# Kernel tuning notes

Measured on AMD Instinct MI355X. Metric: run time of the kernel, lower is better.

The kernel has to match this reference:

```python
import jax, jax.numpy as jnp
import numpy as np

B, S, H, I, E, TOP_K, NS = 2, 2048, 2048, 1408, 8, 2, 2
SI = I * NS  # shared expert intermediate (intermediate_size * num_shared_expert)
INIT = 0.02


def setup_inputs() -> dict:
    key = jax.random.key(0)
    ks = jax.random.split(key, 9)
    f32 = jnp.float32
    return {
        "hidden_states": jax.random.normal(ks[0], (B, S, H), f32),
        # router classifier: Linear(H, E, bias=False), torch weight [E, H]
        "router_w": (jax.random.normal(ks[1], (E, H), f32) * INIT),
        # grouped experts (SwiGLU, no bias): [E, H, I], [E, H, I], [E, I, H]
        "gate_w": (jax.random.normal(ks[2], (E, H, I), f32) * INIT),
        "up_w": (jax.random.normal(ks[3], (E, H, I), f32) * INIT),
        "down_w": (jax.random.normal(ks[4], (E, I, H), f32) * INIT),
        # shared expert _MLP (bias=True), stored in matmul orientation
        "s_gate_w": (jax.random.normal(ks[5], (H, SI), f32) * INIT),
        "s_gate_b": jnp.zeros((SI,), f32),
        "s_up_w": (jax.random.normal(ks[6], (H, SI), f32) * INIT),
        "s_up_b": jnp.zeros((SI,), f32),
        "s_down_w": (jax.random.normal(ks[7], (SI, H), f32) * INIT),
        "s_down_b": jnp.zeros((H,), f32),
    }


def reference(hidden_states, router_w, gate_w, up_w, down_w,
              s_gate_w, s_gate_b, s_up_w, s_up_b, s_down_w, s_down_b):
    b, s, h = hidden_states.shape
    x = hidden_states.reshape(-1, h)          # [T, H]
    T = x.shape[0]
    num_experts = router_w.shape[0]

    # ---- router: logits -> fp32 softmax -> top-k -> renormalize ----
    logits = x @ router_w.T                   # [T, E]
    probs = jax.nn.softmax(logits.astype(jnp.float32), axis=-1)
    topk_w, topk_idx = jax.lax.top_k(probs, TOP_K)            # [T, K]
    topk_w = topk_w / jnp.sum(topk_w, axis=-1, keepdims=True)
    # dense combine weights [T, E]; zero for unrouted experts
    combine = jnp.zeros((T, num_experts), probs.dtype)
    combine = combine.at[jnp.arange(T)[:, None], topk_idx].add(topk_w)

    # ---- grouped SwiGLU experts; scan over E keeps peak memory at [T, I] ----
    def expert_step(acc, ws):
        gw, uw, dw, ce = ws                  # [H,I], [H,I], [I,H], [T]
        out = (jax.nn.silu(x @ gw) * (x @ uw)) @ dw           # [T, H]
        return acc + ce[:, None].astype(out.dtype) * out, None

    moe_out, _ = jax.lax.scan(expert_step, jnp.zeros_like(x),
                              (gate_w, up_w, down_w, combine.T))

    # ---- shared expert SwiGLU MLP (bias=True), overlapped -> added ----
    shared = (jax.nn.silu(x @ s_gate_w + s_gate_b)
              * (x @ s_up_w + s_up_b)) @ s_down_w + s_down_b

    return (moe_out + shared).reshape(b, s, h)
```

## Files before the change

### kernel.cpp

```cpp
#include <hip/hip_runtime.h>
#include <hip/hip_bf16.h>
#include <stdint.h>

#define T_TOK 4096
#define HDIM  2048
#define IDIM  1408
#define NEXP  8
#define SIDIM 2816
#define GU_CAP 781
#define DN_CAP 440

typedef __bf16 bf16_t;
typedef __bf16 bf16x8 __attribute__((ext_vector_type(8)));
typedef __bf16 bf16x4 __attribute__((ext_vector_type(4)));
typedef float  f32x4  __attribute__((ext_vector_type(4)));

typedef uint32_t __attribute__((address_space(3))) lds_u32;
typedef uint32_t __attribute__((address_space(1))) glb_u32;

__device__ __forceinline__ void glds16(const bf16_t* g, const char* l) {
  __builtin_amdgcn_global_load_lds((const glb_u32*)g, (lds_u32*)l, 16, 0, 0);
}

__device__ __forceinline__ void bar() {
  asm volatile("" ::: "memory");
  __builtin_amdgcn_s_barrier();
  asm volatile("" ::: "memory");
}
#define VMW4 asm volatile("s_waitcnt vmcnt(4)" ::: "memory")
#define VMW0 asm volatile("s_waitcnt vmcnt(0)" ::: "memory")

__device__ __forceinline__ int xcd_swz(int orig, int nwg) {
  int q = nwg >> 3, r = nwg & 7;
  int x = orig & 7, i = orig >> 3;
  return (x < r ? x * (q + 1) : r * (q + 1) + (x - r) * q) + i;
}

__global__ void tcvt_kernel(const float* __restrict__ in, bf16_t* __restrict__ out, int R, int C) {
  in  += (size_t)blockIdx.z * R * C;
  out += (size_t)blockIdx.z * R * C;
  __shared__ bf16_t tb[64][72];
  const int r0 = blockIdx.y * 64, c0 = blockIdx.x * 64;
  const int tid = threadIdx.x;
  const int cf4 = tid & 15, rr = tid >> 4;
#pragma unroll
  for (int s = 0; s < 4; ++s) {
    int r = rr + 16 * s;
    float4 v = *(const float4*)(in + (size_t)(r0 + r) * C + c0 + cf4 * 4);
    tb[cf4 * 4 + 0][r] = (bf16_t)v.x;
    tb[cf4 * 4 + 1][r] = (bf16_t)v.y;
    tb[cf4 * 4 + 2][r] = (bf16_t)v.z;
    tb[cf4 * 4 + 3][r] = (bf16_t)v.w;
  }
  __syncthreads();
  const int c = tid >> 2, rb = (tid & 3) * 16;
  bf16x8 w0 = *(const bf16x8*)&tb[c][rb];
  bf16x8 w1 = *(const bf16x8*)&tb[c][rb + 8];
  bf16_t* op = out + (size_t)(c0 + c) * R + r0 + rb;
  *(bf16x8*)op = w0;
  *(bf16x8*)(op + 8) = w1;
}

__global__ void tcvt_gu_kernel(const float* __restrict__ in0, const float* __restrict__ in1,
                               bf16_t* __restrict__ out, int R, int C) {
  const int e = blockIdx.z >> 1, which = blockIdx.z & 1;
  const float* in = (which ? in1 : in0) + (size_t)e * R * C;
  out += (size_t)e * (2 * C) * R;
  __shared__ bf16_t tb[64][72];
  const int r0 = blockIdx.y * 64, c0 = blockIdx.x * 64;
  const int tid = threadIdx.x;
  const int cf4 = tid & 15, rr = tid >> 4;
#pragma unroll
  for (int s = 0; s < 4; ++s) {
    int r = rr + 16 * s;
    float4 v = *(const float4*)(in + (size_t)(r0 + r) * C + c0 + cf4 * 4);
    tb[cf4 * 4 + 0][r] = (bf16_t)v.x;
    tb[cf4 * 4 + 1][r] = (bf16_t)v.y;
    tb[cf4 * 4 + 2][r] = (bf16_t)v.z;
    tb[cf4 * 4 + 3][r] = (bf16_t)v.w;
  }
  __syncthreads();
  const int c = tid >> 2, rb = (tid & 3) * 16;
  bf16x8 w0 = *(const bf16x8*)&tb[c][rb];
  bf16x8 w1 = *(const bf16x8*)&tb[c][rb + 8];
  int cg = c0 + c;
  int nprime = ((cg >> 4) << 5) + which * 16 + (cg & 15);
  bf16_t* op = out + (size_t)nprime * R + r0 + rb;
  *(bf16x8*)op = w0;
  *(bf16x8*)(op + 8) = w1;
}

__global__ void router_kernel(const float* __restrict__ x, const float* __restrict__ rw,
                              bf16_t* __restrict__ xb,
                              int* __restrict__ tk_i, float* __restrict__ tk_w,
                              int* __restrict__ counts) {
  int gtid = blockIdx.x * 256 + threadIdx.x;
  int t = gtid >> 6, lane = gtid & 63;
  const float4* xr = (const float4*)(x + (size_t)t * HDIM);
  bf16x4* xo = (bf16x4*)(xb + (size_t)t * HDIM);
  float acc[NEXP];
#pragma unroll
  for (int e = 0; e < NEXP; e++) acc[e] = 0.f;
  for (int i = lane; i < HDIM / 4; i += 64) {
    float4 xv = xr[i];
    bf16x4 o;
    o[0] = (bf16_t)xv.x; o[1] = (bf16_t)xv.y; o[2] = (bf16_t)xv.z; o[3] = (bf16_t)xv.w;
    xo[i] = o;
#pragma unroll
    for (int e = 0; e < NEXP; e++) {
      float4 wv = ((const float4*)(rw + e * HDIM))[i];
      acc[e] += xv.x * wv.x + xv.y * wv.y + xv.z * wv.z + xv.w * wv.w;
    }
  }
#pragma unroll
  for (int e = 0; e < NEXP; e++)
#pragma unroll
    for (int off = 32; off; off >>= 1) acc[e] += __shfl_down(acc[e], off);
  if (lane == 0) {
    int i1 = 0; float m1 = acc[0];
#pragma unroll
    for (int e = 1; e < NEXP; e++) if (acc[e] > m1) { m1 = acc[e]; i1 = e; }
    int i2 = -1; float m2 = -1e30f;
#pragma unroll
    for (int e = 0; e < NEXP; e++) if (e != i1 && acc[e] > m2) { m2 = acc[e]; i2 = e; }
    float w1 = 1.f / (1.f + __expf(m2 - m1));
    tk_i[t * 2] = i1; tk_i[t * 2 + 1] = i2;
    tk_w[t * 2] = w1; tk_w[t * 2 + 1] = 1.f - w1;
    atomicAdd(&counts[i1], 1); atomicAdd(&counts[i2], 1);
  }
}

__global__ void build_kernel(int* __restrict__ meta) {
  __shared__ int snmt;
  if (threadIdx.x == 0) {
    int o = 0;
    for (int e = 0; e < NEXP; e++) { meta[16 + e] = o; o += meta[e]; }
    meta[24] = o;
    int nmt = 0;
    for (int e = 0; e < NEXP; e++) {
      int nt = (meta[e] + 255) >> 8;
      for (int i = 0; i < nt; i++) { meta[32 + nmt] = e; meta[80 + nmt] = i << 8; nmt++; }
    }
    meta[25] = nmt;
    meta[26] = nmt * 11 + 352;
    meta[27] = nmt * 8 + 128;
    snmt = nmt;
  }
  __syncthreads();
  const int nmt = snmt;
  int4* gt = (int4*)(meta + 128);
  const int ng = nmt * 11 + 352;
  for (int i = threadIdx.x; i < ng; i += 256) {
    int4 v; v.w = 0;
    if (i < nmt * 11) {
      int g = i / (nmt * 2), rem = i - g * (nmt * 2);
      int yt, xt;
      if (g < 5) { yt = rem >> 1; xt = g * 2 + (rem & 1); }
      else       { yt = rem;      xt = 10; }
      v.x = 0 | (meta[32 + yt] << 1); v.y = meta[80 + yt]; v.z = xt * 256;
    } else {
      int k = i - nmt * 11;
      int g = k >> 5, rem = k & 31;
      int yt = rem >> 1, xt = g * 2 + (rem & 1);
      v.x = 1; v.y = yt * 256; v.z = xt * 256;
    }
    gt[i] = v;
  }
  int4* dt4 = (int4*)(meta + 3328);
  const int nd = nmt * 8 + 128;
  for (int i = threadIdx.x; i < nd; i += 256) {
    int4 v; v.w = 0;
    if (i < nmt * 8) {
      int g = i / (nmt * 2), rem = i - g * (nmt * 2);
      int yt = rem >> 1, xt = g * 2 + (rem & 1);
      v.x = 0 | (meta[32 + yt] << 1); v.y = meta[80 + yt]; v.z = xt * 256;
    } else {
      int k = i - nmt * 8;
      int g = k >> 5, rem = k & 31;
      int yt = rem >> 1, xt = g * 2 + (rem & 1);
      v.x = 1; v.y = yt * 256; v.z = xt * 256;
    }
    dt4[i] = v;
  }
}

__global__ void scatter_kernel(const int* __restrict__ tk_i, const float* __restrict__ tk_w,
                               int* __restrict__ meta, int* __restrict__ tok_idx,
                               int* __restrict__ tk_slot) {
  int t = blockIdx.x * 256 + threadIdx.x;
  if (t >= T_TOK) return;
#pragma unroll
  for (int k = 0; k < 2; k++) {
    int e = tk_i[t * 2 + k];
    int pos = meta[16 + e] + atomicAdd(&meta[8 + e], 1);
    tok_idx[pos] = t; tk_slot[t * 2 + k] = pos;
  }
}

template <int OP>
__device__ __forceinline__
void gemm8p_body(const bf16_t* __restrict__ A0, const bf16_t* __restrict__ A1,
                 const bf16_t* __restrict__ B0, const bf16_t* __restrict__ B1,
                 bf16_t* __restrict__ O0, bf16_t* __restrict__ O1,
                 const float* __restrict__ bg, const float* __restrict__ bu,
                 const int* __restrict__ meta, const int* __restrict__ tok_idx) {
  const int ntiles = meta[OP == 0 ? 26 : 27];
  const int l = blockIdx.x;
  if (l >= ntiles) return;
  const int s = xcd_swz(l, ntiles);
  const int4 tv = ((const int4*)(meta + (OP == 0 ? 128 : 3328)))[s];
  const int kind = tv.x & 1, e = (tv.x >> 1) & 7;
  const int row0 = tv.y, n0 = tv.z;

  int cnt, slot0 = 0, strideA, strideB;
  const bf16_t *Ab, *Bp;
  int NKT;
  if (OP == 0) {
    NKT = HDIM / 64;
    strideA = HDIM; strideB = HDIM; Ab = A0;
    if (kind == 0) {
      slot0 = meta[16 + e]; cnt = meta[17 + e] - slot0;
      Bp = B0 + (size_t)e * (2 * IDIM) * HDIM;
    } else { cnt = T_TOK; Bp = B1; }
  } else {
    if (kind == 0) {
      NKT = IDIM / 64;
      slot0 = meta[16 + e]; cnt = meta[17 + e] - slot0;
      Ab = A0; strideA = IDIM;
      Bp = B0 + (size_t)e * HDIM * IDIM; strideB = IDIM;
    } else {
      NKT = SIDIM / 64;
      cnt = T_TOK; Ab = A1; strideA = SIDIM;
      Bp = B1; strideB = SIDIM;
    }
  }

  __shared__ __align__(16) char smem[131072];

  const int t = threadIdx.x;
  const int lane = t & 63, wid = t >> 6;
  const int wr = wid >> 2, wc = wid & 3;
  const int lr = lane & 15, lg = lane >> 4;

  const bf16_t* pA[4]; const bf16_t* pB[4]; int dG[4];
#pragma unroll
  for (int j = 0; j < 4; ++j) {
    int g = j * 512 + t;
    int r = g >> 3;
    int c16 = (g & 7) ^ (r & 7);
    dG[j] = g * 16;
    int rr = row0 + r;
    if (kind == 0 && rr >= cnt) rr = cnt - 1;
    int arow;
    if (OP == 0 && kind == 0) arow = tok_idx[slot0 + rr];
    else if (OP == 1 && kind == 0) arow = slot0 + rr;
    else arow = rr;
    pA[j] = Ab + (size_t)arow * strideA + c16 * 8;
    pB[j] = Bp + (size_t)(n0 + r) * strideB + c16 * 8;
  }

  const int cswz0 = ((lg) ^ (lr & 7)) * 16;
  const int cswz1 = ((4 + lg) ^ (lr & 7)) * 16;
  const int aRowB = (wr * 128 + lr) * 128;
  const int bRowB = (wc * 64 + lr) * 128 + 65536;

  f32x4 acc[8][4];
#pragma unroll
  for (int mi = 0; mi < 8; ++mi)
#pragma unroll
    for (int ni = 0; ni < 4; ++ni) acc[mi][ni] = (f32x4)(0.f);

  bf16x8 aL[4][2], aH[4][2], bL[2][2], bH[2][2];

#define ST_A(BUFO, KT, JH) { \
    glds16(pA[(JH)*2]   + (KT)*64, smem + (BUFO) + dG[(JH)*2]); \
    glds16(pA[(JH)*2+1] + (KT)*64, smem + (BUFO) + dG[(JH)*2+1]); }
#define ST_B(BUFO, KT, JH) { \
    glds16(pB[(JH)*2]   + (KT)*64, smem + 65536 + (BUFO) + dG[(JH)*2]); \
    glds16(pB[(JH)*2+1] + (KT)*64, smem + 65536 + (BUFO) + dG[(JH)*2+1]); }
#define RD_A(af, BUFO, MIH) { \
    _Pragma("unroll") for (int mi = 0; mi < 4; ++mi) { \
      af[mi][0] = *(const bf16x8*)(smem + (BUFO) + aRowB + (MIH)*8192 + mi*2048 + cswz0); \
      af[mi][1] = *(const bf16x8*)(smem + (BUFO) + aRowB + (MIH)*8192 + mi*2048 + cswz1); } }
#define RD_B(bf, BUFO, NIH) { \
    _Pragma("unroll") for (int ni = 0; ni < 2; ++ni) { \
      bf[ni][0] = *(const bf16x8*)(smem + (BUFO) + bRowB + (NIH)*4096 + ni*2048 + cswz0); \
      bf[ni][1] = *(const bf16x8*)(smem + (BUFO) + bRowB + (NIH)*4096 + ni*2048 + cswz1); } }
#define MMQ(af, bf, MO, NO) { \
    __builtin_amdgcn_s_setprio(1); \
    _Pragma("unroll") for (int ni = 0; ni < 2; ++ni) \
    _Pragma("unroll") for (int mi = 0; mi < 4; ++mi) { \
      acc[(MO)+mi][(NO)+ni] = __builtin_amdgcn_mfma_f32_16x16x32_bf16(af[mi][0], bf[ni][0], acc[(MO)+mi][(NO)+ni], 0, 0, 0); \
      acc[(MO)+mi][(NO)+ni] = __builtin_amdgcn_mfma_f32_16x16x32_bf16(af[mi][1], bf[ni][1], acc[(MO)+mi][(NO)+ni], 0, 0, 0); } \
    __builtin_amdgcn_s_setprio(0); }
#define KTILE(KT, BO, NBO, W) { \
    RD_A(aL, BO, 0); RD_B(bL, BO, 0); \
    if ((KT) + 1 < NKT) ST_B(NBO, (KT) + 1, 0); \
    bar(); MMQ(aL, bL, 0, 0); bar(); \
    RD_A(aH, BO, 1); \
    if ((KT) + 1 < NKT) ST_B(NBO, (KT) + 1, 1); \
    bar(); MMQ(aH, bL, 4, 0); bar(); \
    RD_B(bH, BO, 1); \
    if ((KT) + 2 < NKT) ST_A(BO, (KT) + 2, 0); \
    bar(); MMQ(aH, bH, 4, 2); bar(); \
    if ((KT) + 2 < NKT) ST_A(BO, (KT) + 2, 1); \
    bar(); MMQ(aL, bH, 0, 2); \
    W; bar(); }

  ST_A(0, 0, 0); ST_A(0, 0, 1);
  ST_B(0, 0, 0); ST_B(0, 0, 1);
  ST_A(32768, 1, 0); ST_A(32768, 1, 1);
  VMW4; bar();

  for (int kt = 0; kt < NKT - 2; kt += 2) {
    KTILE(kt, 0, 32768, VMW4);
    KTILE(kt + 1, 32768, 0, VMW4);
  }
  KTILE(NKT - 2, 0, 32768, VMW0);
  KTILE(NKT - 1, 32768, 0, VMW0);

  if (OP == 0) {
    bf16_t* Ho = kind ? O1 : O0;
    const int HN = kind ? SIDIM : IDIM;
    const int Lbase = n0 >> 1;
#pragma unroll
    for (int mi = 0; mi < 8; ++mi)
#pragma unroll
      for (int j = 0; j < 4; ++j) {
        int row = wr * 128 + mi * 16 + lg * 4 + j;
        int grow = row0 + row;
        if (kind == 0 && grow >= cnt) continue;
        size_t orow = (size_t)((kind ? 0 : slot0) + grow);
#pragma unroll
        for (int nih = 0; nih < 2; ++nih) {
          int Lr = wc * 32 + nih * 16 + lr;
          float g = acc[mi][2 * nih][j];
          float u = acc[mi][2 * nih + 1][j];
          if (kind) { g += bg[Lbase + Lr]; u += bu[Lbase + Lr]; }
          float h = (g / (1.f + __expf(-g))) * u;
          Ho[orow * HN + Lbase + Lr] = (bf16_t)h;
        }
      }
  } else {
    bf16_t* Po = kind ? O1 : O0;
#pragma unroll
    for (int mi = 0; mi < 8; ++mi)
#pragma unroll
      for (int j = 0; j < 4; ++j) {
        int row = wr * 128 + mi * 16 + lg * 4 + j;
        int grow = row0 + row;
        if (kind == 0 && grow >= cnt) continue;
        size_t orow = (size_t)((kind ? 0 : slot0) + grow);
#pragma unroll
        for (int ni = 0; ni < 4; ++ni) {
          int col = n0 + wc * 64 + ni * 16 + lr;
          Po[orow * HDIM + col] = (bf16_t)acc[mi][ni][j];
        }
      }
  }
#undef ST_A
#undef ST_B
#undef RD_A
#undef RD_B
#undef MMQ
#undef KTILE
}

__global__ __launch_bounds__(512, 2)
void gu_gemm(const bf16_t* A0, const bf16_t* A1, const bf16_t* B0, const bf16_t* B1,
             bf16_t* O0, bf16_t* O1, const float* bg, const float* bu,
             const int* meta, const int* tok_idx) {
  gemm8p_body<0>(A0, A1, B0, B1, O0, O1, bg, bu, meta, tok_idx);
}
__global__ __launch_bounds__(512, 2)
void dn_gemm(const bf16_t* A0, const bf16_t* A1, const bf16_t* B0, const bf16_t* B1,
             bf16_t* O0, bf16_t* O1, const float* bg, const float* bu,
             const int* meta, const int* tok_idx) {
  gemm8p_body<1>(A0, A1, B0, B1, O0, O1, bg, bu, meta, tok_idx);
}

__global__ void combine_kernel(const bf16_t* __restrict__ sh,
                               const bf16_t* __restrict__ rt, const int* __restrict__ tk_slot,
                               const float* __restrict__ tk_w, const float* __restrict__ sdb,
                               float* __restrict__ out) {
  const int t = blockIdx.x;
  const int c = threadIdx.x * 8;
  const int s1 = tk_slot[2 * t], s2 = tk_slot[2 * t + 1];
  const float w1 = tk_w[2 * t], w2 = tk_w[2 * t + 1];
  bf16x8 a = *(const bf16x8*)(sh + (size_t)t * HDIM + c);
  bf16x8 r1 = *(const bf16x8*)(rt + (size_t)s1 * HDIM + c);
  bf16x8 r2 = *(const bf16x8*)(rt + (size_t)s2 * HDIM + c);
  float4 d0 = *(const float4*)(sdb + c);
  float4 d1 = *(const float4*)(sdb + c + 4);
  float o[8];
#pragma unroll
  for (int i = 0; i < 8; i++)
    o[i] = (float)a[i] + w1 * (float)r1[i] + w2 * (float)r2[i];
  o[0] += d0.x; o[1] += d0.y; o[2] += d0.z; o[3] += d0.w;
  o[4] += d1.x; o[5] += d1.y; o[6] += d1.z; o[7] += d1.w;
  float4* op = (float4*)(out + (size_t)t * HDIM + c);
  op[0] = make_float4(o[0], o[1], o[2], o[3]);
  op[1] = make_float4(o[4], o[5], o[6], o[7]);
}

extern "C" void kernel_launch(void* const* d_in, const int* in_sizes, int n_in,
                              void* d_out, int out_size, void* d_ws, size_t ws_size,
                              hipStream_t stream) {
  const float* x_f  = (const float*)d_in[0];
  const float* rw   = (const float*)d_in[1];
  const float* gate = (const float*)d_in[2];
  const float* up   = (const float*)d_in[3];
  const float* down = (const float*)d_in[4];
  const float* sgw  = (const float*)d_in[5];
  const float* sgb  = (const float*)d_in[6];
  const float* suw  = (const float*)d_in[7];
  const float* sub  = (const float*)d_in[8];
  const float* sdw  = (const float*)d_in[9];
  const float* sdb  = (const float*)d_in[10];
  float* out = (float*)d_out;

  char* ws = (char*)d_ws;
  size_t off = 0;
  auto alloc = [&](size_t bytes) {
    char* p = ws + off;
    off += (bytes + 255) & ~(size_t)255;
    return p;
  };
  bf16_t* xb    = (bf16_t*)alloc((size_t)T_TOK * HDIM * 2);
  char*   bgur  = alloc((size_t)NEXP * 2 * IDIM * HDIM * 2);
  bf16_t* BguR  = (bf16_t*)bgur;
  bf16_t* BguS  = (bf16_t*)alloc((size_t)2 * SIDIM * HDIM * 2);
  bf16_t* dT    = (bf16_t*)alloc((size_t)NEXP * HDIM * IDIM * 2);
  bf16_t* sdT   = (bf16_t*)alloc((size_t)HDIM * SIDIM * 2);
  bf16_t* hid_r = (bf16_t*)alloc((size_t)(T_TOK * 2) * IDIM * 2);
  bf16_t* hid_s = (bf16_t*)alloc((size_t)T_TOK * SIDIM * 2);
  int*    meta  = (int*)alloc(32768);
  int*    tok_idx = (int*)alloc(8192 * 4);
  int*    tk_slot = (int*)alloc(8192 * 4);
  int*    tk_i    = (int*)alloc((size_t)T_TOK * 2 * 4);
  float*  tk_w2   = (float*)alloc((size_t)T_TOK * 2 * 4);

  bf16_t* rt_p = (bf16_t*)bgur;
  bf16_t* sh_p = (bf16_t*)(bgur + (size_t)8192 * HDIM * 2);

  hipMemsetAsync(meta, 0, 64, stream);

  tcvt_gu_kernel<<<dim3(IDIM / 64, HDIM / 64, NEXP * 2), 256, 0, stream>>>(
      gate, up, BguR, HDIM, IDIM);
  tcvt_gu_kernel<<<dim3(SIDIM / 64, HDIM / 64, 2), 256, 0, stream>>>(
      sgw, suw, BguS, HDIM, SIDIM);
  tcvt_kernel<<<dim3(HDIM / 64, IDIM / 64, NEXP), 256, 0, stream>>>(down, dT, IDIM, HDIM);
  tcvt_kernel<<<dim3(HDIM / 64, SIDIM / 64, 1), 256, 0, stream>>>(sdw, sdT, SIDIM, HDIM);

  router_kernel<<<T_TOK / 4, 256, 0, stream>>>(x_f, rw, xb, tk_i, tk_w2, meta);
  build_kernel<<<1, 256, 0, stream>>>(meta);
  scatter_kernel<<<T_TOK / 256, 256, 0, stream>>>(tk_i, tk_w2, meta, tok_idx, tk_slot);

  gu_gemm<<<GU_CAP, 512, 0, stream>>>(
      xb, nullptr, BguR, BguS, hid_r, hid_s, sgb, sub, meta, tok_idx);
  dn_gemm<<<DN_CAP, 512, 0, stream>>>(
      hid_r, hid_s, dT, sdT, rt_p, sh_p, nullptr, nullptr, meta, nullptr);
  combine_kernel<<<T_TOK, 256, 0, stream>>>(sh_p, rt_p, tk_slot, tk_w2, sdb, out);
}
```

Before: 622.0 us.

## Use XOR-swizzled fp32 LDS staging in weight transpose and interleave down-GEMM tile order

The weight transpose-convert kernels now stage raw fp32 float4 rows in shared memory using an XOR-swizzled slot layout, then convert to bf16 on readout. This replaces scattered 2-byte bf16 LDS writes, which are meant to suffer from bank conflicts. The two kernels are merged into one template. Separately, the down-GEMM tile table is reordered so each of 8 chunks begins with 16 shared-expert tiles followed by routed tiles, spreading work differently across XCDs.

```diff
diff --git a/kernel.cpp b/kernel.cpp
--- a/kernel.cpp
+++ b/kernel.cpp
@@ -36,55 +36,42 @@
   return (x < r ? x * (q + 1) : r * (q + 1) + (x - r) * q) + i;
 }
 
-__global__ void tcvt_kernel(const float* __restrict__ in, bf16_t* __restrict__ out, int R, int C) {
-  in  += (size_t)blockIdx.z * R * C;
-  out += (size_t)blockIdx.z * R * C;
-  __shared__ bf16_t tb[64][72];
+template <bool GU>
+__global__ void tcvt2_kernel(const float* __restrict__ in0, const float* __restrict__ in1,
+                             bf16_t* __restrict__ out, int R, int C) {
+  int which = 0;
+  const float* in;
+  if (GU) {
+    int e = blockIdx.z >> 1; which = blockIdx.z & 1;
+    in = (which ? in1 : in0) + (size_t)e * R * C;
+    out += (size_t)e * (2 * C) * R;
+  } else {
+    in = in0 + (size_t)blockIdx.z * R * C;
+    out += (size_t)blockIdx.z * R * C;
+  }
+  __shared__ float tf[64 * 64];
   const int r0 = blockIdx.y * 64, c0 = blockIdx.x * 64;
   const int tid = threadIdx.x;
-  const int cf4 = tid & 15, rr = tid >> 4;
+  const int cb = tid & 15, rr = tid >> 4;
 #pragma unroll
   for (int s = 0; s < 4; ++s) {
     int r = rr + 16 * s;
-    float4 v = *(const float4*)(in + (size_t)(r0 + r) * C + c0 + cf4 * 4);
-    tb[cf4 * 4 + 0][r] = (bf16_t)v.x;
-    tb[cf4 * 4 + 1][r] = (bf16_t)v.y;
-    tb[cf4 * 4 + 2][r] = (bf16_t)v.z;
-    tb[cf4 * 4 + 3][r] = (bf16_t)v.w;
+    float4 v = *(const float4*)(in + (size_t)(r0 + r) * C + c0 + cb * 4);
+    int slot = (cb ^ (r & 7) ^ ((r >> 4) << 1)) & 15;
+    *(float4*)&tf[r * 64 + slot * 4] = v;
   }
   __syncthreads();
   const int c = tid >> 2, rb = (tid & 3) * 16;
-  bf16x8 w0 = *(const bf16x8*)&tb[c][rb];
-  bf16x8 w1 = *(const bf16x8*)&tb[c][rb + 8];
-  bf16_t* op = out + (size_t)(c0 + c) * R + r0 + rb;
-  *(bf16x8*)op = w0;
-  *(bf16x8*)(op + 8) = w1;
-}
-
-__global__ void tcvt_gu_kernel(const float* __restrict__ in0, const float* __restrict__ in1,
-                               bf16_t* __restrict__ out, int R, int C) {
-  const int e = blockIdx.z >> 1, which = blockIdx.z & 1;
-  const float* in = (which ? in1 : in0) + (size_t)e * R * C;
-  out += (size_t)e * (2 * C) * R;
-  __shared__ bf16_t tb[64][72];
-  const int r0 = blockIdx.y * 64, c0 = blockIdx.x * 64;
-  const int tid = threadIdx.x;
-  const int cf4 = tid & 15, rr = tid >> 4;
-#pragma unroll
-  for (int s = 0; s < 4; ++s) {
-    int r = rr + 16 * s;
-    float4 v = *(const float4*)(in + (size_t)(r0 + r) * C + c0 + cf4 * 4);
-    tb[cf4 * 4 + 0][r] = (bf16_t)v.x;
-    tb[cf4 * 4 + 1][r] = (bf16_t)v.y;
-    tb[cf4 * 4 + 2][r] = (bf16_t)v.z;
-    tb[cf4 * 4 + 3][r] = (bf16_t)v.w;
-  }
-  __syncthreads();
-  const int c = tid >> 2, rb = (tid & 3) * 16;
-  bf16x8 w0 = *(const bf16x8*)&tb[c][rb];
-  bf16x8 w1 = *(const bf16x8*)&tb[c][rb + 8];
+  bf16x8 w0, w1;
+#pragma unroll
+  for (int i = 0; i < 16; ++i) {
+    int r = rb + i;
+    int slot = ((c >> 2) ^ (r & 7) ^ ((r >> 4) << 1)) & 15;
+    float v = tf[r * 64 + slot * 4 + (c & 3)];
+    if (i < 8) w0[i] = (bf16_t)v; else w1[i - 8] = (bf16_t)v;
+  }
   int cg = c0 + c;
-  int nprime = ((cg >> 4) << 5) + which * 16 + (cg & 15);
+  int nprime = GU ? (((cg >> 4) << 5) + which * 16 + (cg & 15)) : cg;
   bf16_t* op = out + (size_t)nprime * R + r0 + rb;
   *(bf16x8*)op = w0;
   *(bf16x8*)(op + 8) = w1;
@@ -168,17 +155,18 @@
   }
   int4* dt4 = (int4*)(meta + 3328);
   const int nd = nmt * 8 + 128;
+  const int per = nd >> 3;
   for (int i = threadIdx.x; i < nd; i += 256) {
+    int x = i / per, o = i - x * per;
     int4 v; v.w = 0;
-    if (i < nmt * 8) {
-      int g = i / (nmt * 2), rem = i - g * (nmt * 2);
-      int yt = rem >> 1, xt = g * 2 + (rem & 1);
+    if (o < 16) {
+      int j = x * 16 + o;
+      v.x = 1; v.y = (j >> 3) * 256; v.z = (j & 7) * 256;
+    } else {
+      int j = x * nmt + (o - 16);
+      int gx = j / (nmt * 2), rem = j - gx * (nmt * 2);
+      int yt = rem >> 1, xt = gx * 2 + (rem & 1);
       v.x = 0 | (meta[32 + yt] << 1); v.y = meta[80 + yt]; v.z = xt * 256;
-    } else {
-      int k = i - nmt * 8;
-      int g = k >> 5, rem = k & 31;
-      int yt = rem >> 1, xt = g * 2 + (rem & 1);
-      v.x = 1; v.y = yt * 256; v.z = xt * 256;
     }
     dt4[i] = v;
   }
@@ -445,12 +433,14 @@
 
   hipMemsetAsync(meta, 0, 64, stream);
 
-  tcvt_gu_kernel<<<dim3(IDIM / 64, HDIM / 64, NEXP * 2), 256, 0, stream>>>(
+  tcvt2_kernel<true><<<dim3(IDIM / 64, HDIM / 64, NEXP * 2), 256, 0, stream>>>(
       gate, up, BguR, HDIM, IDIM);
-  tcvt_gu_kernel<<<dim3(SIDIM / 64, HDIM / 64, 2), 256, 0, stream>>>(
+  tcvt2_kernel<true><<<dim3(SIDIM / 64, HDIM / 64, 2), 256, 0, stream>>>(
       sgw, suw, BguS, HDIM, SIDIM);
-  tcvt_kernel<<<dim3(HDIM / 64, IDIM / 64, NEXP), 256, 0, stream>>>(down, dT, IDIM, HDIM);
-  tcvt_kernel<<<dim3(HDIM / 64, SIDIM / 64, 1), 256, 0, stream>>>(sdw, sdT, SIDIM, HDIM);
+  tcvt2_kernel<false><<<dim3(HDIM / 64, IDIM / 64, NEXP), 256, 0, stream>>>(
+      down, nullptr, dT, IDIM, HDIM);
+  tcvt2_kernel<false><<<dim3(HDIM / 64, SIDIM / 64, 1), 256, 0, stream>>>(
+      sdw, nullptr, sdT, SIDIM, HDIM);
 
   router_kernel<<<T_TOK / 4, 256, 0, stream>>>(x_f, rw, xb, tk_i, tk_w2, meta);
   build_kernel<<<1, 256, 0, stream>>>(meta);
```

Result: faster. 586.1 us (-5.8%).
